# Kernel optimization log

Measured on AMD Instinct MI355X. Metric: run time of the kernel, lower is better.

Reference implementation:

```python
import jax, jax.numpy as jnp
import numpy as np

# Enformer/Borzoi-style MHA with relative positional bias
B, T, C = 2, 1536, 1536          # batch, seq bins, input channels
H, K, V = 8, 64, 192             # heads, key_size, value_size
F = 32                           # num_position_features (borzoi, asymmetric: 2 * 16 basis)


def setup_inputs() -> dict:
    key = jax.random.key(0)
    ks = jax.random.split(key, 9)
    he = lambda fan_in: (2.0 / fan_in) ** 0.5  # he_normal scale
    return {
        "x": jax.random.normal(ks[0], (B, T, C), jnp.float32),
        "Wq": jax.random.normal(ks[1], (C, H * K), jnp.float32) * he(C),
        "Wk": jax.random.normal(ks[2], (C, H * K), jnp.float32) * he(C),
        "Wv": jax.random.normal(ks[3], (C, H * V), jnp.float32) * he(C),
        "Wr": jax.random.normal(ks[4], (F, H * K), jnp.float32) * he(F),
        "r_w_bias": jax.random.normal(ks[5], (1, H, 1, K), jnp.float32) * 0.02,
        "r_r_bias": jax.random.normal(ks[6], (1, H, 1, K), jnp.float32) * 0.02,
        "Wo": jax.random.normal(ks[7], (H * V, H * V), jnp.float32) * he(H * V),
        "bo": jnp.zeros((H * V,), jnp.float32),
    }


def positional_features(positions):
    """Borzoi central-mask basis, absolute=True, asymmetric -> [L, F]."""
    nb = F // 2
    pow_rate = np.exp(np.log(T + 1) / nb).astype(np.float32)
    center_widths = pow_rate ** jnp.arange(1, nb + 1, dtype=jnp.float32) - 1.0  # [nb]
    sign = jnp.sign(positions)
    abs_pos = jnp.abs(positions)
    emb = (center_widths[None, :] > abs_pos[:, None]).astype(jnp.float32)  # [L, nb]
    return jnp.concatenate([emb, sign[:, None] * emb], axis=-1)  # [L, 2*nb]


def relative_shift(x):
    """[B,H,T,2T-1] -> [B,H,T,T] relative-shift trick (pad, reshape, slice)."""
    b, h, t, l = x.shape
    x = jnp.pad(x, ((0, 0), (0, 0), (0, 0), (1, 0)))      # [b,h,t,l+1]
    x = x.reshape(b, h, l + 1, t)[:, :, 1:, :]             # [b,h,l,t]
    x = x.reshape(b, h, t, l)
    return x[..., :t]


def reference(x, Wq, Wk, Wv, Wr, r_w_bias, r_r_bias, Wo, bo):
    q = (x @ Wq).reshape(B, T, H, K).transpose(0, 2, 1, 3)   # [B,H,T,K]
    k = (x @ Wk).reshape(B, T, H, K).transpose(0, 2, 1, 3)
    v = (x @ Wv).reshape(B, T, H, V).transpose(0, 2, 1, 3)   # [B,H,T,V]
    q = q * (K ** -0.5)  # scaling=True

    distances = jnp.arange(-T + 1, T, dtype=jnp.float32)     # [2T-1]
    pe = positional_features(distances)                       # [2T-1, F]
    rk = (pe @ Wr).reshape(2 * T - 1, H, K)                   # [2T-1, H, K]

    content_logits = jnp.einsum('bhtk,bhsk->bhts', q + r_w_bias, k)   # [B,H,T,T]
    rel_logits = jnp.einsum('bhtk,rhk->bhtr', q + r_r_bias, rk)       # [B,H,T,2T-1]
    logits = content_logits + relative_shift(rel_logits)

    weights = jax.nn.softmax(logits, axis=-1)
    out = jnp.einsum('bhts,bhsv->bhtv', weights, v)          # [B,H,T,V]
    out = out.transpose(0, 2, 1, 3).reshape(B, T, H * V)     # [B,T,H*V]
    return out @ Wo + bo
```

## Files before the change

### kernel.cpp

```cpp
#include <hip/hip_runtime.h>
#include <hip/hip_bf16.h>

typedef __hip_bfloat16 bf16;
typedef unsigned short ushort;
typedef unsigned int uint;
typedef __attribute__((ext_vector_type(8))) short short8;
typedef __attribute__((ext_vector_type(4))) float f32x4;

#define Bsz 2
#define Tn  1536
#define Cn  1536
#define Hn  8
#define Kn  64
#define Vn  192

__device__ __forceinline__ ushort f2bs(float f) {
  union { bf16 h; ushort u; } cv;
  cv.h = __float2bfloat16(f);
  return cv.u;
}
__device__ __forceinline__ float bs2f(ushort u) {
  union { float f; uint v; } cv; cv.v = ((uint)u) << 16; return cv.f;
}

__device__ __forceinline__ void gld_lds16(const ushort* g, ushort* l) {
  __builtin_amdgcn_global_load_lds(
      (const __attribute__((address_space(1))) uint*)g,
      (__attribute__((address_space(3))) uint*)l, 16, 0, 0);
}

__global__ __launch_bounds__(256) void prep(
    const float* __restrict__ x,  const float* __restrict__ Wq,
    const float* __restrict__ Wk, const float* __restrict__ Wv,
    const float* __restrict__ Wo, const float* __restrict__ Wr,
    ushort* __restrict__ xb, ushort* __restrict__ Wt,
    ushort* __restrict__ Wot, ushort* __restrict__ rkb) {
  const int z = blockIdx.z;
  if (z < 4) {
    if (z < 2 && blockIdx.x >= 16) return;
    const float* in = (z == 0) ? Wq : (z == 1) ? Wk : (z == 2) ? Wv : Wo;
    ushort* out = (z == 0) ? Wt : (z == 1) ? Wt + 512 * 1536
                : (z == 2) ? Wt + 1024 * 1536 : Wot;
    const int Cc = (z < 2) ? 512 : 1536;
    __shared__ float tile[32][33];
    const int bx = blockIdx.x * 32;
    const int by = blockIdx.y * 32;
    const int tx = threadIdx.x & 31, ty = threadIdx.x >> 5;
#pragma unroll
    for (int i = 0; i < 32; i += 8)
      tile[ty + i][tx] = in[(size_t)(by + ty + i) * Cc + bx + tx];
    __syncthreads();
#pragma unroll
    for (int i = 0; i < 32; i += 8)
      out[(size_t)(bx + ty + i) * 1536 + by + tx] = f2bs(tile[tx][ty + i]);
  } else if (z == 4) {
    const int n4 = 3072 * 1536 / 4;
    for (int i = (blockIdx.y * 48 + blockIdx.x) * 256 + threadIdx.x; i < n4;
         i += 2304 * 256) {
      float4 v = ((const float4*)x)[i];
      uint2 o;
      o.x = (uint)f2bs(v.x) | ((uint)f2bs(v.y) << 16);
      o.y = (uint)f2bs(v.z) | ((uint)f2bs(v.w) << 16);
      ((uint2*)xb)[i] = o;
    }
  } else {
    for (int u = blockIdx.y * 48 + blockIdx.x; u < 2 * 3071; u += 2304) {
      const int r = u >> 1;
      const int c = (u & 1) * 256 + threadIdx.x;
      const float d = (float)(r - (Tn - 1));
      const float ad = fabsf(d);
      const float sg = (d > 0.f) ? 1.f : ((d < 0.f) ? -1.f : 0.f);
      float acc = 0.f;
#pragma unroll
      for (int i = 0; i < 16; i++) {
        double cw = exp(log((double)(Tn + 1)) * (double)(i + 1) / 16.0) - 1.0;
        if ((float)cw > ad) acc += Wr[i * 512 + c] + sg * Wr[(16 + i) * 512 + c];
      }
      rkb[(size_t)r * 512 + c] = f2bs(acc);
    }
  }
}

__global__ __launch_bounds__(256) void gemm_qkv(
    const ushort* __restrict__ xb, const ushort* __restrict__ Wt,
    ushort* __restrict__ qb, ushort* __restrict__ kb, ushort* __restrict__ vtb) {
  __shared__ ushort Al[128 * 32];
  __shared__ ushort Bl[128 * 32];
  const int tid = threadIdx.x;
  const int w = tid >> 6, lane = tid & 63, quad = lane >> 4, ln = lane & 15;
  const int bm = blockIdx.y * 128, bn = blockIdx.x * 128;
  const int wm = (w & 1) * 64, wn = (w >> 1) * 64;
  f32x4 acc[4][4];
#pragma unroll
  for (int i = 0; i < 4; i++)
#pragma unroll
    for (int j = 0; j < 4; j++) acc[i][j] = (f32x4){0.f, 0.f, 0.f, 0.f};

  for (int k0 = 0; k0 < 1536; k0 += 32) {
    __syncthreads();
#pragma unroll
    for (int st = 0; st < 2; st++) {
      int idx = tid + st * 256;
      int row = idx >> 2, col = (idx & 3) * 8;
      gld_lds16(xb + (size_t)(bm + row) * 1536 + k0 + col, Al + idx * 8);
      gld_lds16(Wt + (size_t)(bn + row) * 1536 + k0 + col, Bl + idx * 8);
    }
    __syncthreads();
    short8 af[4], bfr[4];
#pragma unroll
    for (int t = 0; t < 4; t++) {
      af[t]  = *(const short8*)(Al + (wm + t * 16 + ln) * 32 + quad * 8);
      bfr[t] = *(const short8*)(Bl + (wn + t * 16 + ln) * 32 + quad * 8);
    }
#pragma unroll
    for (int mt = 0; mt < 4; mt++)
#pragma unroll
      for (int nt = 0; nt < 4; nt++)
        acc[mt][nt] = __builtin_amdgcn_mfma_f32_16x16x32_bf16(
            af[mt], bfr[nt], acc[mt][nt], 0, 0, 0);
  }

  if (bn < 512) {
#pragma unroll
    for (int mt = 0; mt < 4; mt++)
#pragma unroll
      for (int nt = 0; nt < 4; nt++)
#pragma unroll
        for (int r = 0; r < 4; r++) {
          int m = bm + wm + mt * 16 + quad * 4 + r;
          int n = bn + wn + nt * 16 + ln;
          qb[(size_t)m * 512 + n] = f2bs(acc[mt][nt][r] * 0.125f);
        }
  } else if (bn < 1024) {
#pragma unroll
    for (int mt = 0; mt < 4; mt++)
#pragma unroll
      for (int nt = 0; nt < 4; nt++)
#pragma unroll
        for (int r = 0; r < 4; r++) {
          int m = bm + wm + mt * 16 + quad * 4 + r;
          int n = bn - 512 + wn + nt * 16 + ln;
          kb[(size_t)m * 512 + n] = f2bs(acc[mt][nt][r]);
        }
  } else {
#pragma unroll
    for (int mt = 0; mt < 4; mt++)
#pragma unroll
      for (int nt = 0; nt < 4; nt++) {
        int vcol = bn - 1024 + wn + nt * 16 + ln;
        int m0 = bm + wm + mt * 16 + quad * 4;
        uint2 val;
        val.x = (uint)f2bs(acc[mt][nt][0]) | ((uint)f2bs(acc[mt][nt][1]) << 16);
        val.y = (uint)f2bs(acc[mt][nt][2]) | ((uint)f2bs(acc[mt][nt][3]) << 16);
        *(uint2*)(vtb + (size_t)vcol * 3072 + m0) = val;
      }
  }
}

__global__ __launch_bounds__(256) void gemm_out(
    const ushort* __restrict__ att, const ushort* __restrict__ Wot,
    const float* __restrict__ bo, float* __restrict__ out) {
  __shared__ ushort Al[128 * 32];
  __shared__ ushort Bl[128 * 32];
  const int tid = threadIdx.x;
  const int w = tid >> 6, lane = tid & 63, quad = lane >> 4, ln = lane & 15;
  const int bm = blockIdx.y * 128, bn = blockIdx.x * 128;
  const int wm = (w & 1) * 64, wn = (w >> 1) * 64;
  f32x4 acc[4][4];
#pragma unroll
  for (int i = 0; i < 4; i++)
#pragma unroll
    for (int j = 0; j < 4; j++) acc[i][j] = (f32x4){0.f, 0.f, 0.f, 0.f};

  for (int k0 = 0; k0 < 1536; k0 += 32) {
    __syncthreads();
#pragma unroll
    for (int st = 0; st < 2; st++) {
      int idx = tid + st * 256;
      int row = idx >> 2, col = (idx & 3) * 8;
      gld_lds16(att + (size_t)(bm + row) * 1536 + k0 + col, Al + idx * 8);
      gld_lds16(Wot + (size_t)(bn + row) * 1536 + k0 + col, Bl + idx * 8);
    }
    __syncthreads();
    short8 af[4], bfr[4];
#pragma unroll
    for (int t = 0; t < 4; t++) {
      af[t]  = *(const short8*)(Al + (wm + t * 16 + ln) * 32 + quad * 8);
      bfr[t] = *(const short8*)(Bl + (wn + t * 16 + ln) * 32 + quad * 8);
    }
#pragma unroll
    for (int mt = 0; mt < 4; mt++)
#pragma unroll
      for (int nt = 0; nt < 4; nt++)
        acc[mt][nt] = __builtin_amdgcn_mfma_f32_16x16x32_bf16(
            af[mt], bfr[nt], acc[mt][nt], 0, 0, 0);
  }
#pragma unroll
  for (int mt = 0; mt < 4; mt++)
#pragma unroll
    for (int nt = 0; nt < 4; nt++)
#pragma unroll
      for (int r = 0; r < 4; r++) {
        int m = bm + wm + mt * 16 + quad * 4 + r;
        int n = bn + wn + nt * 16 + ln;
        out[(size_t)m * 1536 + n] = acc[mt][nt][r] + bo[n];
      }
}

__global__ __launch_bounds__(256, 2) void attn_mfma(
    const ushort* __restrict__ qb, const ushort* __restrict__ kb,
    const ushort* __restrict__ vtb, const ushort* __restrict__ rkb,
    const float* __restrict__ rwb, const float* __restrict__ rrb,
    ushort* __restrict__ op0, ushort* __restrict__ op1,
    float2* __restrict__ mlb) {
  __shared__ __align__(16) char smem[63488];
  ushort* Kl  = (ushort*)smem;
  ushort* RKl = (ushort*)(smem + 8192);
  ushort* Vl  = (ushort*)(smem + 24576);

  const int L  = blockIdx.x + 24 * blockIdx.y + 192 * blockIdx.z;
  const int h  = L & 7;
  const int g  = L >> 3;
  const int bsk = g / 24;
  const int b  = bsk >> 1;
  const int sk = bsk & 1;
  const int t0 = (g - bsk * 24) * 64;
  const int bT = b * Tn;
  const int tid = threadIdx.x;
  const int w = tid >> 6, lane = tid & 63, quad = lane >> 4, ln = lane & 15;

  ushort* prlb = (ushort*)(smem + 49152 + w * 3584);
  ushort* Pp   = (ushort*)(smem + 49152 + w * 3584);

  const int lr  = lane >> 3;
  const int lcx = (lane & 7) ^ lr;

  short8 qw8[2], qr8[2];
  {
    const ushort* qrow = qb + (size_t)(bT + t0 + 16 * w + ln) * 512 + h * 64;
#pragma unroll
    for (int ks = 0; ks < 2; ks++) {
      int k0 = quad * 8 + ks * 32;
#pragma unroll
      for (int e = 0; e < 8; e++) {
        float qv = bs2f(qrow[k0 + e]);
        qw8[ks][e] = (short)f2bs(qv + rwb[h * 64 + k0 + e]);
        qr8[ks][e] = (short)f2bs(qv + rrb[h * 64 + k0 + e]);
      }
    }
  }

  f32x4 Oacc[12];
  float m_i[4], l_i[4];
#pragma unroll
  for (int vt = 0; vt < 12; vt++) Oacc[vt] = (f32x4){0.f, 0.f, 0.f, 0.f};
#pragma unroll
  for (int r = 0; r < 4; r++) { m_i[r] = -1e30f; l_i[r] = 0.f; }

  {
    const int s0 = sk * 768;
    const int Dbase = s0 - t0 + 1472;
#pragma unroll
    for (int i = 0; i < 2; i++) {
      int kc = w * 2 + i, sr = kc * 8 + lr;
      gld_lds16(kb + (size_t)(bT + s0 + sr) * 512 + h * 64 + lcx * 8,
                (ushort*)(smem + kc * 1024) + lane * 8);
    }
#pragma unroll
    for (int i = 0; i < 4; i++) {
      int kc = w * 4 + i, j = kc * 8 + lr;
      int jr = Dbase + j; jr = jr > 3070 ? 3070 : jr;
      gld_lds16(rkb + (size_t)jr * 512 + h * 64 + lcx * 8,
                (ushort*)(smem + 8192 + kc * 1024) + lane * 8);
    }
  }
  __syncthreads();

  for (int ch = 0; ch < 12; ch++) {
    const int s0 = sk * 768 + ch * 64;

#pragma unroll
    for (int i = 0; i < 6; i++) {
      int kc = w * 6 + i, vr = kc * 8 + lr;
      gld_lds16(vtb + (size_t)(h * 192 + vr) * 3072 + bT + s0 + lcx * 8,
                (ushort*)(smem + 24576 + kc * 1024) + lane * 8);
    }

    f32x4 Sacc[4], Pacc[5];
    __builtin_amdgcn_s_setprio(1);
#pragma unroll
    for (int ct = 0; ct < 4; ct++) {
      Sacc[ct] = (f32x4){0.f, 0.f, 0.f, 0.f};
#pragma unroll
      for (int ks = 0; ks < 2; ks++) {
        short8 bfr = *(const short8*)(
            Kl + (16 * ct + ln) * 64 + ((quad + 4 * ks) ^ (ln & 7)) * 8);
        Sacc[ct] = __builtin_amdgcn_mfma_f32_16x16x32_bf16(qw8[ks], bfr, Sacc[ct], 0, 0, 0);
      }
    }
#pragma unroll
    for (int jtl = 0; jtl < 5; jtl++) {
      int jt = 3 - w + jtl;
      Pacc[jtl] = (f32x4){0.f, 0.f, 0.f, 0.f};
#pragma unroll
      for (int ks = 0; ks < 2; ks++) {
        short8 bfr = *(const short8*)(
            RKl + (16 * jt + ln) * 64 + ((quad + 4 * ks) ^ (ln & 7)) * 8);
        Pacc[jtl] = __builtin_amdgcn_mfma_f32_16x16x32_bf16(qr8[ks], bfr, Pacc[jtl], 0, 0, 0);
      }
    }
    __builtin_amdgcn_s_setprio(0);
#pragma unroll
    for (int jtl = 0; jtl < 5; jtl++)
#pragma unroll
      for (int r = 0; r < 4; r++)
        prlb[(4 * quad + r) * 104 + 16 * jtl + ln] = f2bs(Pacc[jtl][r]);

    __syncthreads();

    if (ch < 11) {
      const int s0n = s0 + 64;
      const int Dbasen = s0n - t0 + 1472;
#pragma unroll
      for (int i = 0; i < 2; i++) {
        int kc = w * 2 + i, sr = kc * 8 + lr;
        gld_lds16(kb + (size_t)(bT + s0n + sr) * 512 + h * 64 + lcx * 8,
                  (ushort*)(smem + kc * 1024) + lane * 8);
      }
#pragma unroll
      for (int i = 0; i < 4; i++) {
        int kc = w * 4 + i, j = kc * 8 + lr;
        int jr = Dbasen + j; jr = jr > 3070 ? 3070 : jr;
        gld_lds16(rkb + (size_t)jr * 512 + h * 64 + lcx * 8,
                  (ushort*)(smem + 8192 + kc * 1024) + lane * 8);
      }
    }

    float pS[4][4];
#pragma unroll
    for (int ct = 0; ct < 4; ct++)
#pragma unroll
      for (int r = 0; r < 4; r++) {
        int row = 4 * quad + r;
        pS[ct][r] = Sacc[ct][r] + bs2f(prlb[row * 104 + 16 * ct + ln - row + 15]);
      }
    float alpha[4];
#pragma unroll
    for (int r = 0; r < 4; r++) {
      float mx = fmaxf(fmaxf(pS[0][r], pS[1][r]), fmaxf(pS[2][r], pS[3][r]));
#pragma unroll
      for (int off = 8; off >= 1; off >>= 1) mx = fmaxf(mx, __shfl_xor(mx, off));
      float mnew = fmaxf(m_i[r], mx);
      alpha[r] = __expf(m_i[r] - mnew);
      m_i[r] = mnew;
      float rs = 0.f;
#pragma unroll
      for (int ct = 0; ct < 4; ct++) {
        pS[ct][r] = __expf(pS[ct][r] - mnew);
        rs += pS[ct][r];
      }
#pragma unroll
      for (int off = 8; off >= 1; off >>= 1) rs += __shfl_xor(rs, off);
      l_i[r] = l_i[r] * alpha[r] + rs;
    }
#pragma unroll
    for (int vt = 0; vt < 12; vt++)
#pragma unroll
      for (int r = 0; r < 4; r++) Oacc[vt][r] *= alpha[r];
#pragma unroll
    for (int ct = 0; ct < 4; ct++)
#pragma unroll
      for (int r = 0; r < 4; r++)
        Pp[(4 * quad + r) * 72 + 16 * ct + ln] = f2bs(pS[ct][r]);
    __asm__ volatile("s_waitcnt lgkmcnt(0)" ::: "memory");

    short8 afr[2];
#pragma unroll
    for (int ks = 0; ks < 2; ks++)
      afr[ks] = *(const short8*)(Pp + ln * 72 + quad * 8 + ks * 32);
    __builtin_amdgcn_s_setprio(1);
#pragma unroll
    for (int vt = 0; vt < 12; vt++) {
#pragma unroll
      for (int ks = 0; ks < 2; ks++) {
        short8 bfr = *(const short8*)(
            Vl + (16 * vt + ln) * 64 + ((quad + 4 * ks) ^ (ln & 7)) * 8);
        Oacc[vt] = __builtin_amdgcn_mfma_f32_16x16x32_bf16(afr[ks], bfr, Oacc[vt], 0, 0, 0);
      }
    }
    __builtin_amdgcn_s_setprio(0);

    __syncthreads();
  }

  ushort* op = sk ? op1 : op0;
  float inv[4];
#pragma unroll
  for (int r = 0; r < 4; r++) inv[r] = 1.f / l_i[r];
#pragma unroll
  for (int vt = 0; vt < 12; vt++)
#pragma unroll
    for (int r = 0; r < 4; r++) {
      int t = t0 + 16 * w + 4 * quad + r;
      op[(size_t)(bT + t) * 1536 + h * 192 + 16 * vt + ln] = f2bs(Oacc[vt][r] * inv[r]);
    }
  if (ln == 0) {
#pragma unroll
    for (int r = 0; r < 4; r++) {
      int t = t0 + 16 * w + 4 * quad + r;
      float2 v; v.x = m_i[r]; v.y = l_i[r];
      mlb[((sk * 2 + b) * 8 + h) * 1536 + t] = v;
    }
  }
}

__global__ __launch_bounds__(256) void attn_combine(
    const ushort* __restrict__ op0, const ushort* __restrict__ op1,
    const float2* __restrict__ mlb, ushort* __restrict__ att) {
  int g = blockIdx.x * 256 + threadIdx.x;
  int row = g / 384;
  int c4 = (g - row * 384) * 4;
  int b = row >= 1536;
  int t = row - b * 1536;
  int h = c4 / 192;
  float2 ml0 = mlb[((0 + b) * 8 + h) * 1536 + t];
  float2 ml1 = mlb[((2 + b) * 8 + h) * 1536 + t];
  float M = fmaxf(ml0.x, ml1.x);
  float w0 = __expf(ml0.x - M) * ml0.y;
  float w1 = __expf(ml1.x - M) * ml1.y;
  float inv = 1.f / (w0 + w1);
  w0 *= inv; w1 *= inv;
  size_t off = (size_t)row * 1536 + c4;
  uint2 a = *(const uint2*)(op0 + off);
  uint2 c = *(const uint2*)(op1 + off);
  uint2 o;
  float r0 = w0 * bs2f((ushort)(a.x & 0xffff)) + w1 * bs2f((ushort)(c.x & 0xffff));
  float r1 = w0 * bs2f((ushort)(a.x >> 16))    + w1 * bs2f((ushort)(c.x >> 16));
  float r2 = w0 * bs2f((ushort)(a.y & 0xffff)) + w1 * bs2f((ushort)(c.y & 0xffff));
  float r3 = w0 * bs2f((ushort)(a.y >> 16))    + w1 * bs2f((ushort)(c.y >> 16));
  o.x = (uint)f2bs(r0) | ((uint)f2bs(r1) << 16);
  o.y = (uint)f2bs(r2) | ((uint)f2bs(r3) << 16);
  *(uint2*)(att + off) = o;
}

extern "C" void kernel_launch(void* const* d_in, const int* in_sizes, int n_in,
                              void* d_out, int out_size, void* d_ws, size_t ws_size,
                              hipStream_t stream) {
  const float* x   = (const float*)d_in[0];
  const float* Wq  = (const float*)d_in[1];
  const float* Wk  = (const float*)d_in[2];
  const float* Wv  = (const float*)d_in[3];
  const float* Wr  = (const float*)d_in[4];
  const float* rwb = (const float*)d_in[5];
  const float* rrb = (const float*)d_in[6];
  const float* Wo  = (const float*)d_in[7];
  const float* bo  = (const float*)d_in[8];
  float* out = (float*)d_out;

  char* ws = (char*)d_ws;
  ushort* xb  = (ushort*)ws;
  ushort* op1 = (ushort*)ws;
  ushort* att = (ushort*)ws;
  ushort* Wot = (ushort*)(ws + 9437184);
  ushort* Wt  = (ushort*)(ws + 14155776);
  ushort* op0 = (ushort*)(ws + 14155776);
  ushort* qb  = (ushort*)(ws + 23592960);
  ushort* kb  = (ushort*)(ws + 26738688);
  ushort* vtb = (ushort*)(ws + 29884416);
  ushort* rkb = (ushort*)(ws + 39321600);
  float2* mlb = (float2*)(ws + 42467328);

  prep<<<dim3(48, 48, 6), dim3(256), 0, stream>>>(
      x, Wq, Wk, Wv, Wo, Wr, xb, Wt, Wot, rkb);
  gemm_qkv<<<dim3(20, 24), dim3(256), 0, stream>>>(xb, Wt, qb, kb, vtb);
  attn_mfma<<<dim3(24, 8, 4), dim3(256), 0, stream>>>(
      qb, kb, vtb, rkb, rwb, rrb, op0, op1, mlb);
  attn_combine<<<dim3(4608), dim3(256), 0, stream>>>(op0, op1, mlb, att);
  gemm_out<<<dim3(12, 24), dim3(256), 0, stream>>>(att, Wot, bo, out);
}
```

Baseline: 258.3 us.

## Replace relative-position MFMA with per-row distinct-value table and LUT gather

The positional features take only 33 distinct values across distances, so rk has only 33 distinct rows per head. The change precomputes q·rk for those 33 rows in a new small dgemm kernel, plus a byte LUT mapping each distance to its row index. The attention kernel then gathers the bias from LDS instead of loading rk tiles and running extra MFMAs with a shifted scratch buffer. It also reorganises the K/V load schedule, shrinks LDS and raises launch bounds to 3 blocks per CU, at the cost of an extra kernel launch and irregular LDS gathers.

```diff
diff --git a/kernel.cpp b/kernel.cpp
--- a/kernel.cpp
+++ b/kernel.cpp
@@ -34,7 +34,8 @@
     const float* __restrict__ Wk, const float* __restrict__ Wv,
     const float* __restrict__ Wo, const float* __restrict__ Wr,
     ushort* __restrict__ xb, ushort* __restrict__ Wt,
-    ushort* __restrict__ Wot, ushort* __restrict__ rkb) {
+    ushort* __restrict__ Wot, ushort* __restrict__ rkdb,
+    unsigned char* __restrict__ lutb) {
   const int z = blockIdx.z;
   if (z < 4) {
     if (z < 2 && blockIdx.x >= 16) return;
@@ -64,19 +65,30 @@
       ((uint2*)xb)[i] = o;
     }
   } else {
-    for (int u = blockIdx.y * 48 + blockIdx.x; u < 2 * 3071; u += 2304) {
-      const int r = u >> 1;
-      const int c = (u & 1) * 256 + threadIdx.x;
-      const float d = (float)(r - (Tn - 1));
-      const float ad = fabsf(d);
-      const float sg = (d > 0.f) ? 1.f : ((d < 0.f) ? -1.f : 0.f);
+    const int base = (blockIdx.y * 48 + blockIdx.x) * 256 + threadIdx.x;
+    if (base < 8 * 40 * 64) {
+      const int h = base / 2560, rem = base % 2560, u = rem >> 6, k = rem & 63;
       float acc = 0.f;
+      if (u < 33) {
+        const float sg = (u == 32) ? 0.f : (u < 16 ? 1.f : -1.f);
+        const int c = (u == 32) ? 16 : (u < 16 ? u + 1 : u - 15);
+#pragma unroll
+        for (int i = 0; i < 16; i++)
+          if (i >= 16 - c)
+            acc += Wr[i * 512 + h * 64 + k] + sg * Wr[(16 + i) * 512 + h * 64 + k];
+      }
+      rkdb[h * 2560 + u * 64 + k] = f2bs(acc);
+    } else if (base < 8 * 40 * 64 + 3072) {
+      const int idx = base - 8 * 40 * 64;
+      const int d = idx - 1535;
+      const float ad = fabsf((float)d);
+      int c = 0;
 #pragma unroll
       for (int i = 0; i < 16; i++) {
         double cw = exp(log((double)(Tn + 1)) * (double)(i + 1) / 16.0) - 1.0;
-        if ((float)cw > ad) acc += Wr[i * 512 + c] + sg * Wr[(16 + i) * 512 + c];
-      }
-      rkb[(size_t)r * 512 + c] = f2bs(acc);
+        if ((float)cw > ad) c++;
+      }
+      lutb[idx] = (unsigned char)((d == 0) ? 32 : (d > 0 ? c - 1 : 15 + c));
     }
   }
 }
@@ -157,6 +169,37 @@
   }
 }
 
+__global__ __launch_bounds__(256) void dgemm(
+    const ushort* __restrict__ qb, const float* __restrict__ rrb,
+    const ushort* __restrict__ rkdb, ushort* __restrict__ Db) {
+  const int t0 = blockIdx.x * 64, h = blockIdx.y, b = blockIdx.z;
+  const int t = t0 + (threadIdx.x >> 2), uu = threadIdx.x & 3;
+  const ushort* qrow = qb + (size_t)(b * Tn + t) * 512 + h * 64;
+  float qf[64];
+#pragma unroll
+  for (int k8 = 0; k8 < 8; k8++) {
+    short8 v = *(const short8*)(qrow + k8 * 8);
+#pragma unroll
+    for (int e = 0; e < 8; e++)
+      qf[k8 * 8 + e] = bs2f(f2bs(bs2f((ushort)v[e]) + rrb[h * 64 + k8 * 8 + e]));
+  }
+#pragma unroll
+  for (int j = 0; j < 9; j++) {
+    int u = uu + 4 * j;
+    if (u < 33) {
+      float acc = 0.f;
+#pragma unroll
+      for (int k8 = 0; k8 < 8; k8++) {
+        short8 rv = *(const short8*)(rkdb + h * 2560 + u * 64 + k8 * 8);
+#pragma unroll
+        for (int e = 0; e < 8; e++)
+          acc += qf[k8 * 8 + e] * bs2f((ushort)rv[e]);
+      }
+      Db[((size_t)(b * 8 + h) * 1536 + t) * 40 + u] = f2bs(acc);
+    }
+  }
+}
+
 __global__ __launch_bounds__(256) void gemm_out(
     const ushort* __restrict__ att, const ushort* __restrict__ Wot,
     const float* __restrict__ bo, float* __restrict__ out) {
@@ -207,16 +250,18 @@
       }
 }
 
-__global__ __launch_bounds__(256, 2) void attn_mfma(
+__global__ __launch_bounds__(256, 3) void attn_mfma(
     const ushort* __restrict__ qb, const ushort* __restrict__ kb,
-    const ushort* __restrict__ vtb, const ushort* __restrict__ rkb,
-    const float* __restrict__ rwb, const float* __restrict__ rrb,
+    const ushort* __restrict__ vtb, const ushort* __restrict__ Db,
+    const unsigned char* __restrict__ lutb,
+    const float* __restrict__ rwb,
     ushort* __restrict__ op0, ushort* __restrict__ op1,
     float2* __restrict__ mlb) {
-  __shared__ __align__(16) char smem[63488];
-  ushort* Kl  = (ushort*)smem;
-  ushort* RKl = (ushort*)(smem + 8192);
-  ushort* Vl  = (ushort*)(smem + 24576);
+  __shared__ __align__(16) char smem[50176];
+  ushort* Kl = (ushort*)smem;
+  ushort* Vl = (ushort*)(smem + 8192);
+  ushort* Dl = (ushort*)(smem + 32768);
+  unsigned char* Ll = (unsigned char*)(smem + 37888);
 
   const int L  = blockIdx.x + 24 * blockIdx.y + 192 * blockIdx.z;
   const int h  = L & 7;
@@ -229,37 +274,13 @@
   const int tid = threadIdx.x;
   const int w = tid >> 6, lane = tid & 63, quad = lane >> 4, ln = lane & 15;
 
-  ushort* prlb = (ushort*)(smem + 49152 + w * 3584);
-  ushort* Pp   = (ushort*)(smem + 49152 + w * 3584);
+  ushort* Pp = (ushort*)(smem + 40960 + w * 2304);
 
   const int lr  = lane >> 3;
   const int lcx = (lane & 7) ^ lr;
 
-  short8 qw8[2], qr8[2];
-  {
-    const ushort* qrow = qb + (size_t)(bT + t0 + 16 * w + ln) * 512 + h * 64;
-#pragma unroll
-    for (int ks = 0; ks < 2; ks++) {
-      int k0 = quad * 8 + ks * 32;
-#pragma unroll
-      for (int e = 0; e < 8; e++) {
-        float qv = bs2f(qrow[k0 + e]);
-        qw8[ks][e] = (short)f2bs(qv + rwb[h * 64 + k0 + e]);
-        qr8[ks][e] = (short)f2bs(qv + rrb[h * 64 + k0 + e]);
-      }
-    }
-  }
-
-  f32x4 Oacc[12];
-  float m_i[4], l_i[4];
-#pragma unroll
-  for (int vt = 0; vt < 12; vt++) Oacc[vt] = (f32x4){0.f, 0.f, 0.f, 0.f};
-#pragma unroll
-  for (int r = 0; r < 4; r++) { m_i[r] = -1e30f; l_i[r] = 0.f; }
-
   {
     const int s0 = sk * 768;
-    const int Dbase = s0 - t0 + 1472;
 #pragma unroll
     for (int i = 0; i < 2; i++) {
       int kc = w * 2 + i, sr = kc * 8 + lr;
@@ -267,26 +288,50 @@
                 (ushort*)(smem + kc * 1024) + lane * 8);
     }
 #pragma unroll
-    for (int i = 0; i < 4; i++) {
-      int kc = w * 4 + i, j = kc * 8 + lr;
-      int jr = Dbase + j; jr = jr > 3070 ? 3070 : jr;
-      gld_lds16(rkb + (size_t)jr * 512 + h * 64 + lcx * 8,
-                (ushort*)(smem + 8192 + kc * 1024) + lane * 8);
-    }
-  }
-  __syncthreads();
-
-  for (int ch = 0; ch < 12; ch++) {
-    const int s0 = sk * 768 + ch * 64;
-
-#pragma unroll
     for (int i = 0; i < 6; i++) {
       int kc = w * 6 + i, vr = kc * 8 + lr;
       gld_lds16(vtb + (size_t)(h * 192 + vr) * 3072 + bT + s0 + lcx * 8,
-                (ushort*)(smem + 24576 + kc * 1024) + lane * 8);
-    }
-
-    f32x4 Sacc[4], Pacc[5];
+                (ushort*)(smem + 8192 + kc * 1024) + lane * 8);
+    }
+    const ushort* dsrc = Db + ((size_t)(b * 8 + h) * 1536 + t0) * 40;
+    gld_lds16(dsrc + w * 512 + lane * 8,
+              (ushort*)(smem + 32768 + w * 1024) + lane * 8);
+    if (w == 0)
+      gld_lds16(dsrc + 4 * 512 + lane * 8,
+                (ushort*)(smem + 32768 + 4096) + lane * 8);
+    if (w < 3)
+      gld_lds16((const ushort*)(lutb + w * 1024) + lane * 8,
+                (ushort*)(smem + 37888 + w * 1024) + lane * 8);
+  }
+
+  short8 qw8[2];
+  {
+    const ushort* qrow = qb + (size_t)(bT + t0 + 16 * w + ln) * 512 + h * 64;
+#pragma unroll
+    for (int ks = 0; ks < 2; ks++) {
+      int k0 = quad * 8 + ks * 32;
+#pragma unroll
+      for (int e = 0; e < 8; e++)
+        qw8[ks][e] = (short)f2bs(bs2f(qrow[k0 + e]) + rwb[h * 64 + k0 + e]);
+    }
+  }
+
+  f32x4 Oacc[12];
+  float m_i[4], l_i[4];
+#pragma unroll
+  for (int vt = 0; vt < 12; vt++) Oacc[vt] = (f32x4){0.f, 0.f, 0.f, 0.f};
+#pragma unroll
+  for (int r = 0; r < 4; r++) { m_i[r] = -1e30f; l_i[r] = 0.f; }
+
+  __syncthreads();
+
+  const int ibase = sk * 768 - t0 - 16 * w - 4 * quad + ln + 1535;
+  const int tl0 = 16 * w + 4 * quad;
+
+  for (int ch = 0; ch < 12; ch++) {
+    const int s0 = sk * 768 + ch * 64;
+
+    f32x4 Sacc[4];
     __builtin_amdgcn_s_setprio(1);
 #pragma unroll
     for (int ct = 0; ct < 4; ct++) {
@@ -298,52 +343,30 @@
         Sacc[ct] = __builtin_amdgcn_mfma_f32_16x16x32_bf16(qw8[ks], bfr, Sacc[ct], 0, 0, 0);
       }
     }
-#pragma unroll
-    for (int jtl = 0; jtl < 5; jtl++) {
-      int jt = 3 - w + jtl;
-      Pacc[jtl] = (f32x4){0.f, 0.f, 0.f, 0.f};
-#pragma unroll
-      for (int ks = 0; ks < 2; ks++) {
-        short8 bfr = *(const short8*)(
-            RKl + (16 * jt + ln) * 64 + ((quad + 4 * ks) ^ (ln & 7)) * 8);
-        Pacc[jtl] = __builtin_amdgcn_mfma_f32_16x16x32_bf16(qr8[ks], bfr, Pacc[jtl], 0, 0, 0);
-      }
-    }
     __builtin_amdgcn_s_setprio(0);
-#pragma unroll
-    for (int jtl = 0; jtl < 5; jtl++)
-#pragma unroll
-      for (int r = 0; r < 4; r++)
-        prlb[(4 * quad + r) * 104 + 16 * jtl + ln] = f2bs(Pacc[jtl][r]);
+
+    float pS[4][4];
+#pragma unroll
+    for (int ct = 0; ct < 4; ct++)
+#pragma unroll
+      for (int r = 0; r < 4; r++) {
+        int idx = ibase + 64 * ch + 16 * ct - r;
+        int u = Ll[idx];
+        pS[ct][r] = Sacc[ct][r] + bs2f(Dl[(tl0 + r) * 40 + u]);
+      }
 
     __syncthreads();
 
     if (ch < 11) {
       const int s0n = s0 + 64;
-      const int Dbasen = s0n - t0 + 1472;
 #pragma unroll
       for (int i = 0; i < 2; i++) {
         int kc = w * 2 + i, sr = kc * 8 + lr;
         gld_lds16(kb + (size_t)(bT + s0n + sr) * 512 + h * 64 + lcx * 8,
                   (ushort*)(smem + kc * 1024) + lane * 8);
       }
-#pragma unroll
-      for (int i = 0; i < 4; i++) {
-        int kc = w * 4 + i, j = kc * 8 + lr;
-        int jr = Dbasen + j; jr = jr > 3070 ? 3070 : jr;
-        gld_lds16(rkb + (size_t)jr * 512 + h * 64 + lcx * 8,
-                  (ushort*)(smem + 8192 + kc * 1024) + lane * 8);
-      }
-    }
-
-    float pS[4][4];
-#pragma unroll
-    for (int ct = 0; ct < 4; ct++)
-#pragma unroll
-      for (int r = 0; r < 4; r++) {
-        int row = 4 * quad + r;
-        pS[ct][r] = Sacc[ct][r] + bs2f(prlb[row * 104 + 16 * ct + ln - row + 15]);
-      }
+    }
+
     float alpha[4];
 #pragma unroll
     for (int r = 0; r < 4; r++) {
@@ -391,6 +414,16 @@
     __builtin_amdgcn_s_setprio(0);
 
     __syncthreads();
+
+    if (ch < 11) {
+      const int s0n = s0 + 64;
+#pragma unroll
+      for (int i = 0; i < 6; i++) {
+        int kc = w * 6 + i, vr = kc * 8 + lr;
+        gld_lds16(vtb + (size_t)(h * 192 + vr) * 3072 + bT + s0n + lcx * 8,
+                  (ushort*)(smem + 8192 + kc * 1024) + lane * 8);
+      }
+    }
   }
 
   ushort* op = sk ? op1 : op0;
@@ -467,14 +500,17 @@
   ushort* qb  = (ushort*)(ws + 23592960);
   ushort* kb  = (ushort*)(ws + 26738688);
   ushort* vtb = (ushort*)(ws + 29884416);
-  ushort* rkb = (ushort*)(ws + 39321600);
+  ushort* Db   = (ushort*)(ws + 39321600);
+  unsigned char* lutb = (unsigned char*)(ws + 41287680);
+  ushort* rkdb = (ushort*)(ws + 41290752);
   float2* mlb = (float2*)(ws + 42467328);
 
   prep<<<dim3(48, 48, 6), dim3(256), 0, stream>>>(
-      x, Wq, Wk, Wv, Wo, Wr, xb, Wt, Wot, rkb);
+      x, Wq, Wk, Wv, Wo, Wr, xb, Wt, Wot, rkdb, lutb);
   gemm_qkv<<<dim3(20, 24), dim3(256), 0, stream>>>(xb, Wt, qb, kb, vtb);
+  dgemm<<<dim3(24, 8, 2), dim3(256), 0, stream>>>(qb, rrb, rkdb, Db);
   attn_mfma<<<dim3(24, 8, 4), dim3(256), 0, stream>>>(
-      qb, kb, vtb, rkb, rwb, rrb, op0, op1, mlb);
+      qb, kb, vtb, Db, lutb, rwb, op0, op1, mlb);
   attn_combine<<<dim3(4608), dim3(256), 0, stream>>>(op0, op1, mlb, att);
   gemm_out<<<dim3(12, 24), dim3(256), 0, stream>>>(att, Wot, bo, out);
 }
```

Result: no change. 254.2 us (-1.6%).
